# Optimization experiments

Hardware: AMD Instinct MI355X
Metric: run time of the kernel (lower is better)

## Reference

```python
import jax, jax.numpy as jnp
import numpy as np
from jax import lax

# dims: S=seq_len, B=batch, D=word dim, HE=encoder hidden, HD=decoder hidden,
# E=atomic embedding dim, A=num_atomic, T=max_steps, SOS=start token id
S, B, D = 48, 64, 300
HE, HD, E, A, T, SOS = 300, 256, 50, 128, 50, 1


def _u(key, shape, scale):
    return jax.random.uniform(key, shape, jnp.float32, -scale, scale)


def setup_inputs() -> dict:
    key = jax.random.key(0)
    ks = iter(jax.random.split(key, 64))
    inp = {"word_vectors": jax.random.normal(next(ks), (S, B, D), jnp.float32)}
    se = 1.0 / np.sqrt(HE)
    for l, din in ((0, D), (1, 2 * HE)):
        for d in ("f", "b"):
            inp[f"e{l}{d}_Wih"] = _u(next(ks), (3 * HE, din), se)
            inp[f"e{l}{d}_Whh"] = _u(next(ks), (3 * HE, HE), se)
            inp[f"e{l}{d}_bih"] = _u(next(ks), (3 * HE,), se)
            inp[f"e{l}{d}_bhh"] = _u(next(ks), (3 * HE,), se)
    sd = 1.0 / np.sqrt(HD)
    for l, din in ((0, E), (1, HD)):
        inp[f"d{l}_Wih"] = _u(next(ks), (3 * HD, din), sd)
        inp[f"d{l}_Whh"] = _u(next(ks), (3 * HD, HD), sd)
        inp[f"d{l}_bih"] = _u(next(ks), (3 * HD,), sd)
        inp[f"d{l}_bhh"] = _u(next(ks), (3 * HD,), sd)
    emb = jax.random.normal(next(ks), (A, E), jnp.float32)
    inp["emb"] = emb.at[0].set(0.0)  # padding_idx=0
    inp["Wout"] = _u(next(ks), (A, HD), sd)
    inp["bout"] = _u(next(ks), (A,), sd)
    so = 1.0 / np.sqrt(D)
    inp["Wh0"] = _u(next(ks), (2 * HD, D), so)
    inp["bh0"] = _u(next(ks), (2 * HD,), so)
    return inp


def gru_cell(x, h, Wih, Whh, bih, bhh):
    # PyTorch GRU cell semantics
    gi = x @ Wih.T + bih
    gh = h @ Whh.T + bhh
    ir, iz, inn = jnp.split(gi, 3, axis=-1)
    hr, hz, hn = jnp.split(gh, 3, axis=-1)
    r = jax.nn.sigmoid(ir + hr)
    z = jax.nn.sigmoid(iz + hz)
    n = jnp.tanh(inn + r * hn)
    return (1.0 - z) * n + z * h


def gru_layer(xs, Wih, Whh, bih, bhh, reverse=False):
    # xs: [S, B, din] -> [S, B, H]; h0 = zeros (torch default)
    h0 = jnp.zeros((xs.shape[1], Whh.shape[1]), xs.dtype)
    def step(h, x):
        hn = gru_cell(x, h, Wih, Whh, bih, bhh)
        return hn, hn
    _, ys = lax.scan(step, h0, xs, reverse=reverse)
    return ys


def reference(word_vectors, e0f_Wih, e0f_Whh, e0f_bih, e0f_bhh, e0b_Wih, e0b_Whh, e0b_bih, e0b_bhh, e1f_Wih, e1f_Whh, e1f_bih, e1f_bhh, e1b_Wih, e1b_Whh, e1b_bih, e1b_bhh, d0_Wih, d0_Whh, d0_bih, d0_bhh, d1_Wih, d1_Whh, d1_bih, d1_bhh, emb, Wout, bout, Wh0, bh0):
    # --- encoder: 2-layer bidirectional GRU (eval mode: no dropout) ---
    x0f = gru_layer(word_vectors, e0f_Wih, e0f_Whh, e0f_bih, e0f_bhh, reverse=False)
    x0b = gru_layer(word_vectors, e0b_Wih, e0b_Whh, e0b_bih, e0b_bhh, reverse=True)
    x0 = jnp.concatenate([x0f, x0b], axis=-1)  # [S,B,2*HE]
    x1f = gru_layer(x0, e1f_Wih, e1f_Whh, e1f_bih, e1f_bhh, reverse=False)
    x1b = gru_layer(x0, e1b_Wih, e1b_Whh, e1b_bih, e1b_bhh, reverse=True)
    enc = x1f + x1b  # view(S,B,2,HE).sum(dim=2) of concat == sum of directions

    N = S * B
    h = jnp.tanh(enc @ Wh0.T + bh0).reshape(N, 2, HD)  # [N,2,HD]
    h0, h1 = h[:, 0], h[:, 1]
    e = jnp.broadcast_to(emb[SOS], (N, E))

    def step(carry, _):
        h0, h1, e = carry
        h0n = gru_cell(e, h0, d0_Wih, d0_Whh, d0_bih, d0_bhh)
        h1n = gru_cell(h0n, h1, d1_Wih, d1_Whh, d1_bih, d1_bhh)
        y = jax.nn.log_softmax(h1n @ Wout.T + bout, axis=-1)  # [N,A]
        p = jnp.argmax(y, axis=-1)
        return (h0n, h1n, emb[p]), y

    _, Y = lax.scan(step, (h0, h1, e), None, length=T)  # [T,N,A]
    return Y.reshape(T, S, B, A)[:-1]
```

## Files before the change

kernel.cpp:

```cpp
#include <hip/hip_runtime.h>
#include <math.h>

#define S_ 48
#define B_ 64
#define D_ 300
#define HE_ 300
#define HD_ 256
#define E_ 50
#define A_ 128
#define T_ 50
#define N_ (S_*B_)
#define NR 6

__device__ __forceinline__ float sigm(float x){ return 1.0f/(1.0f + expf(-x)); }

template<int MODE>
__global__ __launch_bounds__(256)
void gemm_bias_kernel(const float* __restrict__ A, const float* __restrict__ W,
                      const float* __restrict__ bias, float* __restrict__ C,
                      float* __restrict__ C2, int M, int N, int K)
{
  __shared__ float As[16][64];
  __shared__ float Ws[16][64];
  const int tid = threadIdx.x;
  const int bm = blockIdx.y * 64;
  const int bn = blockIdx.x * 64;
  const int tx = tid & 15, ty = tid >> 4;
  const int lr = tid >> 2;
  const int lk = (tid & 3) << 2;
  float acc[4][4] = {{0.f}};
  for (int kb = 0; kb < K; kb += 16) {
    {
      const int row = bm + lr;
      const int k = kb + lk;
      const float* ap = A + (size_t)row * K + k;
      float4 v = make_float4(0.f,0.f,0.f,0.f);
      if (k + 3 < K) v = *reinterpret_cast<const float4*>(ap);
      else {
        if (k   < K) v.x = ap[0];
        if (k+1 < K) v.y = ap[1];
        if (k+2 < K) v.z = ap[2];
        if (k+3 < K) v.w = ap[3];
      }
      As[lk][lr]=v.x; As[lk+1][lr]=v.y; As[lk+2][lr]=v.z; As[lk+3][lr]=v.w;
    }
    {
      const int col = bn + lr;
      const int k = kb + lk;
      float4 v = make_float4(0.f,0.f,0.f,0.f);
      if (col < N) {
        const float* wp = W + (size_t)col * K + k;
        if (k + 3 < K) v = *reinterpret_cast<const float4*>(wp);
        else {
          if (k   < K) v.x = wp[0];
          if (k+1 < K) v.y = wp[1];
          if (k+2 < K) v.z = wp[2];
          if (k+3 < K) v.w = wp[3];
        }
      }
      Ws[lk][lr]=v.x; Ws[lk+1][lr]=v.y; Ws[lk+2][lr]=v.z; Ws[lk+3][lr]=v.w;
    }
    __syncthreads();
    #pragma unroll
    for (int kk = 0; kk < 16; ++kk) {
      float4 a4 = *reinterpret_cast<const float4*>(&As[kk][ty<<2]);
      float4 w4 = *reinterpret_cast<const float4*>(&Ws[kk][tx<<2]);
      const float* a = reinterpret_cast<const float*>(&a4);
      const float* w = reinterpret_cast<const float*>(&w4);
      #pragma unroll
      for (int i = 0; i < 4; ++i)
        #pragma unroll
        for (int j = 0; j < 4; ++j)
          acc[i][j] = fmaf(a[i], w[j], acc[i][j]);
    }
    __syncthreads();
  }
  #pragma unroll
  for (int i = 0; i < 4; ++i) {
    const int m = bm + (ty<<2) + i;
    #pragma unroll
    for (int j = 0; j < 4; ++j) {
      const int n = bn + (tx<<2) + j;
      if (n < N) {
        float v = acc[i][j] + bias[n];
        if (MODE == 0) {
          C[(size_t)m*N + n] = v;
        } else {
          v = tanhf(v);
          if (n < HD_) C[(size_t)m*HD_ + n] = v;
          else         C2[(size_t)m*HD_ + (n-HD_)] = v;
        }
      }
    }
  }
}

__device__ __forceinline__ void tile_mac(const float (*As)[64], const float (*Ws)[16][36],
                                         int tcol, int trow,
                                         float* accr, float* accz, float* accn)
{
  #pragma unroll
  for (int kk = 0; kk < 32; kk += 4) {
    float4 wr4 = *reinterpret_cast<const float4*>(&Ws[0][tcol][kk]);
    float4 wz4 = *reinterpret_cast<const float4*>(&Ws[1][tcol][kk]);
    float4 wn4 = *reinterpret_cast<const float4*>(&Ws[2][tcol][kk]);
    const float* wr = reinterpret_cast<const float*>(&wr4);
    const float* wz = reinterpret_cast<const float*>(&wz4);
    const float* wn = reinterpret_cast<const float*>(&wn4);
    #pragma unroll
    for (int u = 0; u < 4; ++u) {
      float4 a4 = *reinterpret_cast<const float4*>(&As[kk+u][trow]);
      const float* a = reinterpret_cast<const float*>(&a4);
      #pragma unroll
      for (int q = 0; q < 4; ++q) {
        accr[q] = fmaf(a[q], wr[u], accr[q]);
        accz[q] = fmaf(a[q], wz[u], accz[q]);
        accn[q] = fmaf(a[q], wn[u], accn[q]);
      }
    }
  }
}

__global__ __launch_bounds__(256)
void enc_step_kernel(const float* __restrict__ gi_f, const float* __restrict__ gi_b,
                     const float* __restrict__ Whh_f, const float* __restrict__ Whh_b,
                     const float* __restrict__ bhh_f, const float* __restrict__ bhh_b,
                     const float* __restrict__ hin_f, float* __restrict__ hout_f,
                     const float* __restrict__ hin_b, float* __restrict__ hout_b,
                     float* __restrict__ out, int t, int layer)
{
  const int dir = blockIdx.z;
  const float* gi  = dir ? gi_b  : gi_f;
  const float* W   = dir ? Whh_b : Whh_f;
  const float* bhh = dir ? bhh_b : bhh_f;
  const float* hin = dir ? hin_b : hin_f;
  float* hout = dir ? hout_b : hout_f;
  const int tt = dir ? (S_-1 - t) : t;

  __shared__ float As[32][64];
  __shared__ float Ws[3][16][36];
  const int tid = threadIdx.x;
  const int bn = blockIdx.x * 16;
  const int tcol = tid & 15;
  const int trow = (tid >> 4) << 2;
  float accr[4]={0,0,0,0}, accz[4]={0,0,0,0}, accn[4]={0,0,0,0};

  for (int kb = 0; kb < HE_; kb += 32) {
    __syncthreads();
    #pragma unroll
    for (int j = 0; j < 2; ++j) {
      int i = tid + j*256;
      int row = i >> 3;
      int k = (i & 7) << 2;
      const float* ap = hin + (size_t)row*HE_ + kb + k;
      float4 v = make_float4(0.f,0.f,0.f,0.f);
      if (kb + k + 3 < HE_) v = *reinterpret_cast<const float4*>(ap);
      else {
        if (kb+k   < HE_) v.x = ap[0];
        if (kb+k+1 < HE_) v.y = ap[1];
        if (kb+k+2 < HE_) v.z = ap[2];
        if (kb+k+3 < HE_) v.w = ap[3];
      }
      As[k  ][row] = v.x; As[k+1][row] = v.y; As[k+2][row] = v.z; As[k+3][row] = v.w;
    }
    #pragma unroll
    for (int j = 0; j < 6; ++j) {
      int i = tid + j*256;
      int g = i >> 9;
      int c = (i >> 5) & 15;
      int k = i & 31;
      float v = 0.0f;
      if (bn + c < HE_ && kb + k < HE_) v = W[(size_t)(g*HE_ + bn + c)*HE_ + kb + k];
      Ws[g][c][k] = v;
    }
    __syncthreads();
    tile_mac(As, Ws, tcol, trow, accr, accz, accn);
  }

  const int jcol = bn + tcol;
  if (jcol < HE_) {
    #pragma unroll
    for (int i = 0; i < 4; ++i) {
      const int row = trow + i;
      const size_t gbase = (size_t)(tt*B_ + row) * (3*HE_);
      float gr = gi[gbase + jcol];
      float gz = gi[gbase + HE_ + jcol];
      float gn = gi[gbase + 2*HE_ + jcol];
      float r = sigm(gr + accr[i] + bhh[jcol]);
      float z = sigm(gz + accz[i] + bhh[HE_ + jcol]);
      float n = tanhf(gn + r*(accn[i] + bhh[2*HE_ + jcol]));
      float ho = hin[(size_t)row*HE_ + jcol];
      float hn = (1.0f - z)*n + z*ho;
      hout[(size_t)row*HE_ + jcol] = hn;
      if (layer == 0) out[(size_t)(tt*B_ + row)*(2*HE_) + dir*HE_ + jcol] = hn;
      else            out[(size_t)(tt*B_ + row)*HE_ + jcol] += hn;
    }
  }
}

__global__ __launch_bounds__(256)
void transpose_kernel(const float* __restrict__ in, float* __restrict__ out,
                      int NC, int NK)
{
  int idx = blockIdx.x * 256 + threadIdx.x;
  if (idx < NC*NK) {
    int cI = idx / NK, kI = idx % NK;
    out[(size_t)kI*NC + cI] = in[idx];
  }
}

__global__ __launch_bounds__(512, 2)
void dec_persistent(const float* __restrict__ WihT0,
                    const float* __restrict__ WhhT0,
                    const float* __restrict__ WihT1,
                    const float* __restrict__ WhhT1,
                    const float* __restrict__ WoutT,
                    const float* __restrict__ bih0, const float* __restrict__ bhh0,
                    const float* __restrict__ bih1, const float* __restrict__ bhh1,
                    const float* __restrict__ bout,
                    const float* __restrict__ emb,
                    const float* __restrict__ h0init, const float* __restrict__ h1init,
                    float* __restrict__ Y)
{
  __shared__ float h0s[12][256];
  __shared__ float h1s[12][256];
  __shared__ float es[12][52];
  const int tid = threadIdx.x;
  const int bb = blockIdx.x;
  const int R0 = bb * 12;
  const int c  = tid & 255;
  const int half = tid >> 8;
  const int r0 = half * NR;

  for (int i = tid; i < 12*64; i += 512) {
    int r = i >> 6;
    int k = (i & 63) << 2;
    *reinterpret_cast<float4*>(&h0s[r][k]) =
        *reinterpret_cast<const float4*>(&h0init[(size_t)(R0+r)*HD_ + k]);
    *reinterpret_cast<float4*>(&h1s[r][k]) =
        *reinterpret_cast<const float4*>(&h1init[(size_t)(R0+r)*HD_ + k]);
  }
  for (int i = tid; i < 12*E_; i += 512) {
    int r = i / E_, k = i % E_;
    es[r][k] = emb[E_ + k];
  }
  const float b0r = bih0[c] + bhh0[c];
  const float b0z = bih0[HD_+c] + bhh0[HD_+c];
  const float b0ni = bih0[2*HD_+c];
  const float b0nh = bhh0[2*HD_+c];
  const float b1r = bih1[c] + bhh1[c];
  const float b1z = bih1[HD_+c] + bhh1[HD_+c];
  const float b1ni = bih1[2*HD_+c];
  const float b1nh = bhh1[2*HD_+c];
  const float bo0 = bout[tid & 63];
  const float bo1 = bout[64 + (tid & 63)];
  __syncthreads();

  for (int s = 0; s < T_-1; ++s) {
    float ar[NR], az[NR], ani[NR], anh[NR];
    #pragma unroll
    for (int r = 0; r < NR; ++r) { ar[r]=0.f; az[r]=0.f; ani[r]=0.f; anh[r]=0.f; }
    for (int k = 0; k < E_; k += 2) {
      const float* wk = WihT0 + (size_t)k*768;
      float wr0=wk[c],     wz0=wk[HD_+c],     wn0=wk[2*HD_+c];
      float wr1=wk[768+c], wz1=wk[768+HD_+c], wn1=wk[768+2*HD_+c];
      #pragma unroll
      for (int r = 0; r < NR; ++r) {
        float2 x = *reinterpret_cast<const float2*>(&es[r0+r][k]);
        ar[r]=fmaf(x.x,wr0,ar[r]);  ar[r]=fmaf(x.y,wr1,ar[r]);
        az[r]=fmaf(x.x,wz0,az[r]);  az[r]=fmaf(x.y,wz1,az[r]);
        ani[r]=fmaf(x.x,wn0,ani[r]); ani[r]=fmaf(x.y,wn1,ani[r]);
      }
    }
    for (int k = 0; k < HD_; k += 4) {
      float wr[4], wz[4], wn[4];
      #pragma unroll
      for (int u = 0; u < 4; ++u) {
        const float* wk = WhhT0 + (size_t)(k+u)*768;
        wr[u]=wk[c]; wz[u]=wk[HD_+c]; wn[u]=wk[2*HD_+c];
      }
      #pragma unroll
      for (int r = 0; r < NR; ++r) {
        float4 x = *reinterpret_cast<const float4*>(&h0s[r0+r][k]);
        ar[r]=fmaf(x.x,wr[0],ar[r]); ar[r]=fmaf(x.y,wr[1],ar[r]);
        ar[r]=fmaf(x.z,wr[2],ar[r]); ar[r]=fmaf(x.w,wr[3],ar[r]);
        az[r]=fmaf(x.x,wz[0],az[r]); az[r]=fmaf(x.y,wz[1],az[r]);
        az[r]=fmaf(x.z,wz[2],az[r]); az[r]=fmaf(x.w,wz[3],az[r]);
        anh[r]=fmaf(x.x,wn[0],anh[r]); anh[r]=fmaf(x.y,wn[1],anh[r]);
        anh[r]=fmaf(x.z,wn[2],anh[r]); anh[r]=fmaf(x.w,wn[3],anh[r]);
      }
    }
    __syncthreads();
    {
      float hnew[NR];
      #pragma unroll
      for (int r = 0; r < NR; ++r) {
        float rg = sigm(ar[r] + b0r);
        float zg = sigm(az[r] + b0z);
        float ng = tanhf(ani[r] + b0ni + rg*(anh[r] + b0nh));
        float hold = h0s[r0+r][c];
        hnew[r] = (1.0f - zg)*ng + zg*hold;
      }
      #pragma unroll
      for (int r = 0; r < NR; ++r) h0s[r0+r][c] = hnew[r];
    }
    __syncthreads();
    #pragma unroll
    for (int r = 0; r < NR; ++r) { ar[r]=0.f; az[r]=0.f; ani[r]=0.f; anh[r]=0.f; }
    for (int k = 0; k < HD_; k += 4) {
      float wr[4], wz[4], wn[4];
      #pragma unroll
      for (int u = 0; u < 4; ++u) {
        const float* wk = WihT1 + (size_t)(k+u)*768;
        wr[u]=wk[c]; wz[u]=wk[HD_+c]; wn[u]=wk[2*HD_+c];
      }
      #pragma unroll
      for (int r = 0; r < NR; ++r) {
        float4 x = *reinterpret_cast<const float4*>(&h0s[r0+r][k]);
        ar[r]=fmaf(x.x,wr[0],ar[r]); ar[r]=fmaf(x.y,wr[1],ar[r]);
        ar[r]=fmaf(x.z,wr[2],ar[r]); ar[r]=fmaf(x.w,wr[3],ar[r]);
        az[r]=fmaf(x.x,wz[0],az[r]); az[r]=fmaf(x.y,wz[1],az[r]);
        az[r]=fmaf(x.z,wz[2],az[r]); az[r]=fmaf(x.w,wz[3],az[r]);
        ani[r]=fmaf(x.x,wn[0],ani[r]); ani[r]=fmaf(x.y,wn[1],ani[r]);
        ani[r]=fmaf(x.z,wn[2],ani[r]); ani[r]=fmaf(x.w,wn[3],ani[r]);
      }
    }
    for (int k = 0; k < HD_; k += 4) {
      float wr[4], wz[4], wn[4];
      #pragma unroll
      for (int u = 0; u < 4; ++u) {
        const float* wk = WhhT1 + (size_t)(k+u)*768;
        wr[u]=wk[c]; wz[u]=wk[HD_+c]; wn[u]=wk[2*HD_+c];
      }
      #pragma unroll
      for (int r = 0; r < NR; ++r) {
        float4 x = *reinterpret_cast<const float4*>(&h1s[r0+r][k]);
        ar[r]=fmaf(x.x,wr[0],ar[r]); ar[r]=fmaf(x.y,wr[1],ar[r]);
        ar[r]=fmaf(x.z,wr[2],ar[r]); ar[r]=fmaf(x.w,wr[3],ar[r]);
        az[r]=fmaf(x.x,wz[0],az[r]); az[r]=fmaf(x.y,wz[1],az[r]);
        az[r]=fmaf(x.z,wz[2],az[r]); az[r]=fmaf(x.w,wz[3],az[r]);
        anh[r]=fmaf(x.x,wn[0],anh[r]); anh[r]=fmaf(x.y,wn[1],anh[r]);
        anh[r]=fmaf(x.z,wn[2],anh[r]); anh[r]=fmaf(x.w,wn[3],anh[r]);
      }
    }
    __syncthreads();
    {
      float hnew[NR];
      #pragma unroll
      for (int r = 0; r < NR; ++r) {
        float rg = sigm(ar[r] + b1r);
        float zg = sigm(az[r] + b1z);
        float ng = tanhf(ani[r] + b1ni + rg*(anh[r] + b1nh));
        float hold = h1s[r0+r][c];
        hnew[r] = (1.0f - zg)*ng + zg*hold;
      }
      #pragma unroll
      for (int r = 0; r < NR; ++r) h1s[r0+r][c] = hnew[r];
    }
    __syncthreads();
    {
      const int w = tid >> 6;
      const int lane = tid & 63;
      if (w < 6) {
        const int row0 = 2*w;
        float a00=0.f, a01=0.f, a10=0.f, a11=0.f;
        for (int k = 0; k < HD_; k += 2) {
          float w00 = WoutT[(size_t)k*A_ + lane];
          float w01 = WoutT[(size_t)k*A_ + 64 + lane];
          float w10 = WoutT[(size_t)(k+1)*A_ + lane];
          float w11 = WoutT[(size_t)(k+1)*A_ + 64 + lane];
          float2 hv0 = *reinterpret_cast<const float2*>(&h1s[row0][k]);
          float2 hv1 = *reinterpret_cast<const float2*>(&h1s[row0+1][k]);
          a00 = fmaf(hv0.x, w00, a00); a00 = fmaf(hv0.y, w10, a00);
          a01 = fmaf(hv0.x, w01, a01); a01 = fmaf(hv0.y, w11, a01);
          a10 = fmaf(hv1.x, w00, a10); a10 = fmaf(hv1.y, w10, a10);
          a11 = fmaf(hv1.x, w01, a11); a11 = fmaf(hv1.y, w11, a11);
        }
        float va[2][2] = {{a00,a01},{a10,a11}};
        #pragma unroll
        for (int rr = 0; rr < 2; ++rr) {
          const int row = row0 + rr;
          float v0 = va[rr][0] + bo0;
          float v1 = va[rr][1] + bo1;
          float mx = fmaxf(v0, v1);
          #pragma unroll
          for (int off = 32; off >= 1; off >>= 1) mx = fmaxf(mx, __shfl_xor(mx, off));
          float sum = expf(v0 - mx) + expf(v1 - mx);
          #pragma unroll
          for (int off = 32; off >= 1; off >>= 1) sum += __shfl_xor(sum, off);
          float lz = mx + logf(sum);
          float* Yr = Y + ((size_t)s*N_ + R0 + row)*A_;
          Yr[lane]      = v0 - lz;
          Yr[64 + lane] = v1 - lz;
          float bv; int bi;
          if (v0 >= v1) { bv = v0; bi = lane; } else { bv = v1; bi = 64 + lane; }
          #pragma unroll
          for (int off = 32; off >= 1; off >>= 1) {
            float ov = __shfl_xor(bv, off);
            int   oi = __shfl_xor(bi, off);
            if (ov > bv || (ov == bv && oi < bi)) { bv = ov; bi = oi; }
          }
          if (lane < E_) es[row][lane] = emb[(size_t)bi*E_ + lane];
        }
      }
    }
    __syncthreads();
  }
}

extern "C" void kernel_launch(void* const* d_in, const int* in_sizes, int n_in,
                              void* d_out, int out_size, void* d_ws, size_t ws_size,
                              hipStream_t stream)
{
  (void)in_sizes; (void)n_in; (void)out_size; (void)ws_size;
  const float* wv      = (const float*)d_in[0];
  const float* e0f_Wih = (const float*)d_in[1];
  const float* e0f_Whh = (const float*)d_in[2];
  const float* e0f_bih = (const float*)d_in[3];
  const float* e0f_bhh = (const float*)d_in[4];
  const float* e0b_Wih = (const float*)d_in[5];
  const float* e0b_Whh = (const float*)d_in[6];
  const float* e0b_bih = (const float*)d_in[7];
  const float* e0b_bhh = (const float*)d_in[8];
  const float* e1f_Wih = (const float*)d_in[9];
  const float* e1f_Whh = (const float*)d_in[10];
  const float* e1f_bih = (const float*)d_in[11];
  const float* e1f_bhh = (const float*)d_in[12];
  const float* e1b_Wih = (const float*)d_in[13];
  const float* e1b_Whh = (const float*)d_in[14];
  const float* e1b_bih = (const float*)d_in[15];
  const float* e1b_bhh = (const float*)d_in[16];
  const float* d0_Wih  = (const float*)d_in[17];
  const float* d0_Whh  = (const float*)d_in[18];
  const float* d0_bih  = (const float*)d_in[19];
  const float* d0_bhh  = (const float*)d_in[20];
  const float* d1_Wih  = (const float*)d_in[21];
  const float* d1_Whh  = (const float*)d_in[22];
  const float* d1_bih  = (const float*)d_in[23];
  const float* d1_bhh  = (const float*)d_in[24];
  const float* emb     = (const float*)d_in[25];
  const float* Wout    = (const float*)d_in[26];
  const float* bout    = (const float*)d_in[27];
  const float* Wh0     = (const float*)d_in[28];
  const float* bh0     = (const float*)d_in[29];

  float* ws = (float*)d_ws;
  size_t off = 0;
  auto alloc = [&](size_t n){ float* q = ws + off; off += n; return q; };
  float* giA = alloc((size_t)N_*3*HE_);
  float* giB = alloc((size_t)N_*3*HE_);
  float* x0  = alloc((size_t)N_*2*HE_);
  float* enc = alloc((size_t)N_*HE_);
  float* hfA = alloc((size_t)B_*HE_);
  float* hfB = alloc((size_t)B_*HE_);
  float* hbA = alloc((size_t)B_*HE_);
  float* hbB = alloc((size_t)B_*HE_);
  float* h0A = giA;
  float* h1A = giA + (size_t)N_*HD_;
  float* WihT0 = x0;
  float* WhhT0 = WihT0 + (size_t)E_*768;
  float* WihT1 = WhhT0 + (size_t)HD_*768;
  float* WhhT1 = WihT1 + (size_t)HD_*768;
  float* WoutT = WhhT1 + (size_t)HD_*768;
  float* Y = (float*)d_out;

  const dim3 blk(256);

  gemm_bias_kernel<0><<<dim3(15,48), blk, 0, stream>>>(wv, e0f_Wih, e0f_bih, giA, nullptr, N_, 3*HE_, D_);
  gemm_bias_kernel<0><<<dim3(15,48), blk, 0, stream>>>(wv, e0b_Wih, e0b_bih, giB, nullptr, N_, 3*HE_, D_);
  hipMemsetAsync(hfA, 0, (size_t)B_*HE_*sizeof(float), stream);
  hipMemsetAsync(hbA, 0, (size_t)B_*HE_*sizeof(float), stream);
  {
    float* hfi = hfA; float* hfo = hfB; float* hbi = hbA; float* hbo = hbB;
    for (int t = 0; t < S_; ++t) {
      enc_step_kernel<<<dim3(19,1,2), blk, 0, stream>>>(giA, giB, e0f_Whh, e0b_Whh,
          e0f_bhh, e0b_bhh, hfi, hfo, hbi, hbo, x0, t, 0);
      float* tmp = hfi; hfi = hfo; hfo = tmp;
      tmp = hbi; hbi = hbo; hbo = tmp;
    }
  }
  gemm_bias_kernel<0><<<dim3(15,48), blk, 0, stream>>>(x0, e1f_Wih, e1f_bih, giA, nullptr, N_, 3*HE_, 2*HE_);
  gemm_bias_kernel<0><<<dim3(15,48), blk, 0, stream>>>(x0, e1b_Wih, e1b_bih, giB, nullptr, N_, 3*HE_, 2*HE_);
  hipMemsetAsync(hfA, 0, (size_t)B_*HE_*sizeof(float), stream);
  hipMemsetAsync(hbA, 0, (size_t)B_*HE_*sizeof(float), stream);
  hipMemsetAsync(enc, 0, (size_t)N_*HE_*sizeof(float), stream);
  {
    float* hfi = hfA; float* hfo = hfB; float* hbi = hbA; float* hbo = hbB;
    for (int t = 0; t < S_; ++t) {
      enc_step_kernel<<<dim3(19,1,2), blk, 0, stream>>>(giA, giB, e1f_Whh, e1b_Whh,
          e1f_bhh, e1b_bhh, hfi, hfo, hbi, hbo, enc, t, 1);
      float* tmp = hfi; hfi = hfo; hfo = tmp;
      tmp = hbi; hbi = hbo; hbo = tmp;
    }
  }
  gemm_bias_kernel<1><<<dim3(8,48), blk, 0, stream>>>(enc, Wh0, bh0, h0A, h1A, N_, 2*HD_, HE_);
  transpose_kernel<<<dim3(150), blk, 0, stream>>>(d0_Wih, WihT0, 3*HD_, E_);
  transpose_kernel<<<dim3(768), blk, 0, stream>>>(d0_Whh, WhhT0, 3*HD_, HD_);
  transpose_kernel<<<dim3(768), blk, 0, stream>>>(d1_Wih, WihT1, 3*HD_, HD_);
  transpose_kernel<<<dim3(768), blk, 0, stream>>>(d1_Whh, WhhT1, 3*HD_, HD_);
  transpose_kernel<<<dim3(128), blk, 0, stream>>>(Wout,   WoutT, A_,    HD_);
  dec_persistent<<<dim3(N_/12), dim3(512), 0, stream>>>(
      WihT0, WhhT0, WihT1, WhhT1, WoutT,
      d0_bih, d0_bhh, d1_bih, d1_bhh, bout,
      emb, h0A, h1A, Y);
}
```

Measured before the change: 6.856 ms.

## Run each encoder GRU layer as one persistent kernel and merge decoder matvec loops

```diff
diff --git a/kernel.cpp b/kernel.cpp
--- a/kernel.cpp
+++ b/kernel.cpp
@@ -10,13 +10,13 @@
 #define A_ 128
 #define T_ 50
 #define N_ (S_*B_)
-#define NR 6
 
 __device__ __forceinline__ float sigm(float x){ return 1.0f/(1.0f + expf(-x)); }
 
 template<int MODE>
 __global__ __launch_bounds__(256)
-void gemm_bias_kernel(const float* __restrict__ A, const float* __restrict__ W,
+void gemm_bias_kernel(const float* __restrict__ A, const float* __restrict__ A2,
+                      const float* __restrict__ W,
                       const float* __restrict__ bias, float* __restrict__ C,
                       float* __restrict__ C2, int M, int N, int K)
 {
@@ -42,6 +42,18 @@
         if (k+2 < K) v.z = ap[2];
         if (k+3 < K) v.w = ap[3];
       }
+      if (MODE == 2) {
+        const float* ap2 = A2 + (size_t)row * K + k;
+        if (k + 3 < K) {
+          float4 v2 = *reinterpret_cast<const float4*>(ap2);
+          v.x += v2.x; v.y += v2.y; v.z += v2.z; v.w += v2.w;
+        } else {
+          if (k   < K) v.x += ap2[0];
+          if (k+1 < K) v.y += ap2[1];
+          if (k+2 < K) v.z += ap2[2];
+          if (k+3 < K) v.w += ap2[3];
+        }
+      }
       As[lk][lr]=v.x; As[lk+1][lr]=v.y; As[lk+2][lr]=v.z; As[lk+3][lr]=v.w;
     }
     {
@@ -95,121 +107,91 @@
   }
 }
 
-__device__ __forceinline__ void tile_mac(const float (*As)[64], const float (*Ws)[16][36],
-                                         int tcol, int trow,
-                                         float* accr, float* accz, float* accn)
-{
-  #pragma unroll
-  for (int kk = 0; kk < 32; kk += 4) {
-    float4 wr4 = *reinterpret_cast<const float4*>(&Ws[0][tcol][kk]);
-    float4 wz4 = *reinterpret_cast<const float4*>(&Ws[1][tcol][kk]);
-    float4 wn4 = *reinterpret_cast<const float4*>(&Ws[2][tcol][kk]);
-    const float* wr = reinterpret_cast<const float*>(&wr4);
-    const float* wz = reinterpret_cast<const float*>(&wz4);
-    const float* wn = reinterpret_cast<const float*>(&wn4);
-    #pragma unroll
-    for (int u = 0; u < 4; ++u) {
-      float4 a4 = *reinterpret_cast<const float4*>(&As[kk+u][trow]);
-      const float* a = reinterpret_cast<const float*>(&a4);
-      #pragma unroll
-      for (int q = 0; q < 4; ++q) {
-        accr[q] = fmaf(a[q], wr[u], accr[q]);
-        accz[q] = fmaf(a[q], wz[u], accz[q]);
-        accn[q] = fmaf(a[q], wn[u], accn[q]);
-      }
-    }
-  }
-}
-
-__global__ __launch_bounds__(256)
-void enc_step_kernel(const float* __restrict__ gi_f, const float* __restrict__ gi_b,
-                     const float* __restrict__ Whh_f, const float* __restrict__ Whh_b,
-                     const float* __restrict__ bhh_f, const float* __restrict__ bhh_b,
-                     const float* __restrict__ hin_f, float* __restrict__ hout_f,
-                     const float* __restrict__ hin_b, float* __restrict__ hout_b,
-                     float* __restrict__ out, int t, int layer)
-{
-  const int dir = blockIdx.z;
-  const float* gi  = dir ? gi_b  : gi_f;
-  const float* W   = dir ? Whh_b : Whh_f;
-  const float* bhh = dir ? bhh_b : bhh_f;
-  const float* hin = dir ? hin_b : hin_f;
-  float* hout = dir ? hout_b : hout_f;
-  const int tt = dir ? (S_-1 - t) : t;
-
-  __shared__ float As[32][64];
-  __shared__ float Ws[3][16][36];
-  const int tid = threadIdx.x;
-  const int bn = blockIdx.x * 16;
-  const int tcol = tid & 15;
-  const int trow = (tid >> 4) << 2;
-  float accr[4]={0,0,0,0}, accz[4]={0,0,0,0}, accn[4]={0,0,0,0};
-
-  for (int kb = 0; kb < HE_; kb += 32) {
-    __syncthreads();
-    #pragma unroll
-    for (int j = 0; j < 2; ++j) {
-      int i = tid + j*256;
-      int row = i >> 3;
-      int k = (i & 7) << 2;
-      const float* ap = hin + (size_t)row*HE_ + kb + k;
-      float4 v = make_float4(0.f,0.f,0.f,0.f);
-      if (kb + k + 3 < HE_) v = *reinterpret_cast<const float4*>(ap);
-      else {
-        if (kb+k   < HE_) v.x = ap[0];
-        if (kb+k+1 < HE_) v.y = ap[1];
-        if (kb+k+2 < HE_) v.z = ap[2];
-        if (kb+k+3 < HE_) v.w = ap[3];
-      }
-      As[k  ][row] = v.x; As[k+1][row] = v.y; As[k+2][row] = v.z; As[k+3][row] = v.w;
-    }
-    #pragma unroll
-    for (int j = 0; j < 6; ++j) {
-      int i = tid + j*256;
-      int g = i >> 9;
-      int c = (i >> 5) & 15;
-      int k = i & 31;
-      float v = 0.0f;
-      if (bn + c < HE_ && kb + k < HE_) v = W[(size_t)(g*HE_ + bn + c)*HE_ + kb + k];
-      Ws[g][c][k] = v;
-    }
-    __syncthreads();
-    tile_mac(As, Ws, tcol, trow, accr, accz, accn);
-  }
-
-  const int jcol = bn + tcol;
-  if (jcol < HE_) {
-    #pragma unroll
-    for (int i = 0; i < 4; ++i) {
-      const int row = trow + i;
-      const size_t gbase = (size_t)(tt*B_ + row) * (3*HE_);
-      float gr = gi[gbase + jcol];
-      float gz = gi[gbase + HE_ + jcol];
-      float gn = gi[gbase + 2*HE_ + jcol];
-      float r = sigm(gr + accr[i] + bhh[jcol]);
-      float z = sigm(gz + accz[i] + bhh[HE_ + jcol]);
-      float n = tanhf(gn + r*(accn[i] + bhh[2*HE_ + jcol]));
-      float ho = hin[(size_t)row*HE_ + jcol];
-      float hn = (1.0f - z)*n + z*ho;
-      hout[(size_t)row*HE_ + jcol] = hn;
-      if (layer == 0) out[(size_t)(tt*B_ + row)*(2*HE_) + dir*HE_ + jcol] = hn;
-      else            out[(size_t)(tt*B_ + row)*HE_ + jcol] += hn;
-    }
-  }
-}
-
 __global__ __launch_bounds__(256)
 void transpose_kernel(const float* __restrict__ in, float* __restrict__ out,
-                      int NC, int NK)
+                      int NC, int NK, int NKP)
 {
   int idx = blockIdx.x * 256 + threadIdx.x;
-  if (idx < NC*NK) {
-    int cI = idx / NK, kI = idx % NK;
-    out[(size_t)kI*NC + cI] = in[idx];
+  if (idx < NC*NKP) {
+    int cI = idx / NKP, kI = idx % NKP;
+    out[(size_t)kI*NC + cI] = (kI < NK) ? in[(size_t)cI*NK + kI] : 0.0f;
   }
 }
 
-__global__ __launch_bounds__(512, 2)
+template<int LAYER>
+__global__ __launch_bounds__(640)
+void enc_layer_persistent(const float* __restrict__ gi_f, const float* __restrict__ gi_b,
+                          const float* __restrict__ WhhT_f, const float* __restrict__ WhhT_b,
+                          const float* __restrict__ bhh_f, const float* __restrict__ bhh_b,
+                          float* __restrict__ out, float* __restrict__ outB)
+{
+  const int dir = blockIdx.y;
+  const float* gi  = dir ? gi_b   : gi_f;
+  const float* WT  = dir ? WhhT_b : WhhT_f;
+  const float* bhh = dir ? bhh_b  : bhh_f;
+  float* o = (LAYER == 1 && dir) ? outB : out;
+
+  __shared__ float hA[8][304];
+  __shared__ float hB[8][304];
+  const int tid = threadIdx.x;
+  const int half = tid / 320;
+  const int j = tid - half*320;
+  const int R0 = blockIdx.x * 8;
+  const int r0 = half * 4;
+  const bool act = (j < HE_);
+
+  float b_r = 0.f, b_z = 0.f, b_n = 0.f;
+  if (act) { b_r = bhh[j]; b_z = bhh[HE_+j]; b_n = bhh[2*HE_+j]; }
+  __syncthreads();
+
+  for (int t = 0; t < S_; ++t) {
+    const int tt = dir ? (S_-1 - t) : t;
+    float (*hin)[304]  = (t & 1) ? hB : hA;
+    float (*hout)[304] = (t & 1) ? hA : hB;
+    float ar[4]={0,0,0,0}, az[4]={0,0,0,0}, an[4]={0,0,0,0};
+    if (act && t > 0) {
+      for (int k = 0; k < HE_; k += 4) {
+        float wr[4], wz[4], wn[4];
+        #pragma unroll
+        for (int u = 0; u < 4; ++u) {
+          const float* wk = WT + (size_t)(k+u)*(3*HE_);
+          wr[u] = wk[j]; wz[u] = wk[HE_+j]; wn[u] = wk[2*HE_+j];
+        }
+        #pragma unroll
+        for (int r = 0; r < 4; ++r) {
+          float4 h4 = *reinterpret_cast<const float4*>(&hin[r0+r][k]);
+          ar[r]=fmaf(h4.x,wr[0],ar[r]); ar[r]=fmaf(h4.y,wr[1],ar[r]);
+          ar[r]=fmaf(h4.z,wr[2],ar[r]); ar[r]=fmaf(h4.w,wr[3],ar[r]);
+          az[r]=fmaf(h4.x,wz[0],az[r]); az[r]=fmaf(h4.y,wz[1],az[r]);
+          az[r]=fmaf(h4.z,wz[2],az[r]); az[r]=fmaf(h4.w,wz[3],az[r]);
+          an[r]=fmaf(h4.x,wn[0],an[r]); an[r]=fmaf(h4.y,wn[1],an[r]);
+          an[r]=fmaf(h4.z,wn[2],an[r]); an[r]=fmaf(h4.w,wn[3],an[r]);
+        }
+      }
+    }
+    if (act) {
+      #pragma unroll
+      for (int r = 0; r < 4; ++r) {
+        const int row = R0 + r0 + r;
+        const size_t gb = (size_t)(tt*B_ + row) * (3*HE_);
+        float gr = gi[gb + j];
+        float gz = gi[gb + HE_ + j];
+        float gn = gi[gb + 2*HE_ + j];
+        float rg = sigm(gr + ar[r] + b_r);
+        float zg = sigm(gz + az[r] + b_z);
+        float ng = tanhf(gn + rg*(an[r] + b_n));
+        float ho = (t > 0) ? hin[r0+r][j] : 0.0f;
+        float hn = (1.0f - zg)*ng + zg*ho;
+        hout[r0+r][j] = hn;
+        if (LAYER == 0) o[(size_t)(tt*B_ + row)*(2*HE_) + dir*HE_ + j] = hn;
+        else            o[(size_t)(tt*B_ + row)*HE_ + j] = hn;
+      }
+    }
+    __syncthreads();
+  }
+}
+
+__global__ __launch_bounds__(512)
 void dec_persistent(const float* __restrict__ WihT0,
                     const float* __restrict__ WhhT0,
                     const float* __restrict__ WihT1,
@@ -226,23 +208,21 @@
   __shared__ float h1s[12][256];
   __shared__ float es[12][52];
   const int tid = threadIdx.x;
-  const int bb = blockIdx.x;
-  const int R0 = bb * 12;
+  const int R0 = blockIdx.x * 12;
   const int c  = tid & 255;
   const int half = tid >> 8;
-  const int r0 = half * NR;
+  const int r0 = half * 6;
 
   for (int i = tid; i < 12*64; i += 512) {
-    int r = i >> 6;
-    int k = (i & 63) << 2;
+    int r = i >> 6, k = (i & 63) << 2;
     *reinterpret_cast<float4*>(&h0s[r][k]) =
         *reinterpret_cast<const float4*>(&h0init[(size_t)(R0+r)*HD_ + k]);
     *reinterpret_cast<float4*>(&h1s[r][k]) =
         *reinterpret_cast<const float4*>(&h1init[(size_t)(R0+r)*HD_ + k]);
   }
-  for (int i = tid; i < 12*E_; i += 512) {
-    int r = i / E_, k = i % E_;
-    es[r][k] = emb[E_ + k];
+  for (int i = tid; i < 12*52; i += 512) {
+    int r = i / 52, k = i - r*52;
+    es[r][k] = (k < E_) ? emb[E_ + k] : 0.0f;
   }
   const float b0r = bih0[c] + bhh0[c];
   const float b0z = bih0[HD_+c] + bhh0[HD_+c];
@@ -257,30 +237,18 @@
   __syncthreads();
 
   for (int s = 0; s < T_-1; ++s) {
-    float ar[NR], az[NR], ani[NR], anh[NR];
-    #pragma unroll
-    for (int r = 0; r < NR; ++r) { ar[r]=0.f; az[r]=0.f; ani[r]=0.f; anh[r]=0.f; }
-    for (int k = 0; k < E_; k += 2) {
-      const float* wk = WihT0 + (size_t)k*768;
-      float wr0=wk[c],     wz0=wk[HD_+c],     wn0=wk[2*HD_+c];
-      float wr1=wk[768+c], wz1=wk[768+HD_+c], wn1=wk[768+2*HD_+c];
-      #pragma unroll
-      for (int r = 0; r < NR; ++r) {
-        float2 x = *reinterpret_cast<const float2*>(&es[r0+r][k]);
-        ar[r]=fmaf(x.x,wr0,ar[r]);  ar[r]=fmaf(x.y,wr1,ar[r]);
-        az[r]=fmaf(x.x,wz0,az[r]);  az[r]=fmaf(x.y,wz1,az[r]);
-        ani[r]=fmaf(x.x,wn0,ani[r]); ani[r]=fmaf(x.y,wn1,ani[r]);
-      }
-    }
-    for (int k = 0; k < HD_; k += 4) {
+    float ar[6]={0,0,0,0,0,0}, az[6]={0,0,0,0,0,0};
+    float ani[6]={0,0,0,0,0,0}, anh[6]={0,0,0,0,0,0};
+    for (int kq = 0; kq < 64; ++kq) {
+      const int k = kq << 2;
       float wr[4], wz[4], wn[4];
       #pragma unroll
       for (int u = 0; u < 4; ++u) {
         const float* wk = WhhT0 + (size_t)(k+u)*768;
-        wr[u]=wk[c]; wz[u]=wk[HD_+c]; wn[u]=wk[2*HD_+c];
-      }
-      #pragma unroll
-      for (int r = 0; r < NR; ++r) {
+        wr[u]=wk[c]; wz[u]=wk[256+c]; wn[u]=wk[512+c];
+      }
+      #pragma unroll
+      for (int r = 0; r < 6; ++r) {
         float4 x = *reinterpret_cast<const float4*>(&h0s[r0+r][k]);
         ar[r]=fmaf(x.x,wr[0],ar[r]); ar[r]=fmaf(x.y,wr[1],ar[r]);
         ar[r]=fmaf(x.z,wr[2],ar[r]); ar[r]=fmaf(x.w,wr[3],ar[r]);
@@ -289,12 +257,30 @@
         anh[r]=fmaf(x.x,wn[0],anh[r]); anh[r]=fmaf(x.y,wn[1],anh[r]);
         anh[r]=fmaf(x.z,wn[2],anh[r]); anh[r]=fmaf(x.w,wn[3],anh[r]);
       }
+      if (kq < 13) {
+        float vr[4], vz[4], vn[4];
+        #pragma unroll
+        for (int u = 0; u < 4; ++u) {
+          const float* wk = WihT0 + (size_t)(k+u)*768;
+          vr[u]=wk[c]; vz[u]=wk[256+c]; vn[u]=wk[512+c];
+        }
+        #pragma unroll
+        for (int r = 0; r < 6; ++r) {
+          float4 e = *reinterpret_cast<const float4*>(&es[r0+r][k]);
+          ar[r]=fmaf(e.x,vr[0],ar[r]); ar[r]=fmaf(e.y,vr[1],ar[r]);
+          ar[r]=fmaf(e.z,vr[2],ar[r]); ar[r]=fmaf(e.w,vr[3],ar[r]);
+          az[r]=fmaf(e.x,vz[0],az[r]); az[r]=fmaf(e.y,vz[1],az[r]);
+          az[r]=fmaf(e.z,vz[2],az[r]); az[r]=fmaf(e.w,vz[3],az[r]);
+          ani[r]=fmaf(e.x,vn[0],ani[r]); ani[r]=fmaf(e.y,vn[1],ani[r]);
+          ani[r]=fmaf(e.z,vn[2],ani[r]); ani[r]=fmaf(e.w,vn[3],ani[r]);
+        }
+      }
     }
     __syncthreads();
     {
-      float hnew[NR];
-      #pragma unroll
-      for (int r = 0; r < NR; ++r) {
+      float hnew[6];
+      #pragma unroll
+      for (int r = 0; r < 6; ++r) {
         float rg = sigm(ar[r] + b0r);
         float zg = sigm(az[r] + b0z);
         float ng = tanhf(ani[r] + b0ni + rg*(anh[r] + b0nh));
@@ -302,52 +288,44 @@
         hnew[r] = (1.0f - zg)*ng + zg*hold;
       }
       #pragma unroll
-      for (int r = 0; r < NR; ++r) h0s[r0+r][c] = hnew[r];
+      for (int r = 0; r < 6; ++r) h0s[r0+r][c] = hnew[r];
     }
     __syncthreads();
     #pragma unroll
-    for (int r = 0; r < NR; ++r) { ar[r]=0.f; az[r]=0.f; ani[r]=0.f; anh[r]=0.f; }
-    for (int k = 0; k < HD_; k += 4) {
-      float wr[4], wz[4], wn[4];
+    for (int r = 0; r < 6; ++r) { ar[r]=0.f; az[r]=0.f; ani[r]=0.f; anh[r]=0.f; }
+    for (int kq = 0; kq < 64; ++kq) {
+      const int k = kq << 2;
+      float vr[4], vz[4], vn[4], wr[4], wz[4], wn[4];
       #pragma unroll
       for (int u = 0; u < 4; ++u) {
-        const float* wk = WihT1 + (size_t)(k+u)*768;
-        wr[u]=wk[c]; wz[u]=wk[HD_+c]; wn[u]=wk[2*HD_+c];
-      }
-      #pragma unroll
-      for (int r = 0; r < NR; ++r) {
+        const float* wk  = WihT1 + (size_t)(k+u)*768;
+        vr[u]=wk[c]; vz[u]=wk[256+c]; vn[u]=wk[512+c];
+        const float* wk2 = WhhT1 + (size_t)(k+u)*768;
+        wr[u]=wk2[c]; wz[u]=wk2[256+c]; wn[u]=wk2[512+c];
+      }
+      #pragma unroll
+      for (int r = 0; r < 6; ++r) {
         float4 x = *reinterpret_cast<const float4*>(&h0s[r0+r][k]);
-        ar[r]=fmaf(x.x,wr[0],ar[r]); ar[r]=fmaf(x.y,wr[1],ar[r]);
-        ar[r]=fmaf(x.z,wr[2],ar[r]); ar[r]=fmaf(x.w,wr[3],ar[r]);
-        az[r]=fmaf(x.x,wz[0],az[r]); az[r]=fmaf(x.y,wz[1],az[r]);
-        az[r]=fmaf(x.z,wz[2],az[r]); az[r]=fmaf(x.w,wz[3],az[r]);
-        ani[r]=fmaf(x.x,wn[0],ani[r]); ani[r]=fmaf(x.y,wn[1],ani[r]);
-        ani[r]=fmaf(x.z,wn[2],ani[r]); ani[r]=fmaf(x.w,wn[3],ani[r]);
-      }
-    }
-    for (int k = 0; k < HD_; k += 4) {
-      float wr[4], wz[4], wn[4];
-      #pragma unroll
-      for (int u = 0; u < 4; ++u) {
-        const float* wk = WhhT1 + (size_t)(k+u)*768;
-        wr[u]=wk[c]; wz[u]=wk[HD_+c]; wn[u]=wk[2*HD_+c];
-      }
-      #pragma unroll
-      for (int r = 0; r < NR; ++r) {
-        float4 x = *reinterpret_cast<const float4*>(&h1s[r0+r][k]);
-        ar[r]=fmaf(x.x,wr[0],ar[r]); ar[r]=fmaf(x.y,wr[1],ar[r]);
-        ar[r]=fmaf(x.z,wr[2],ar[r]); ar[r]=fmaf(x.w,wr[3],ar[r]);
-        az[r]=fmaf(x.x,wz[0],az[r]); az[r]=fmaf(x.y,wz[1],az[r]);
-        az[r]=fmaf(x.z,wz[2],az[r]); az[r]=fmaf(x.w,wz[3],az[r]);
-        anh[r]=fmaf(x.x,wn[0],anh[r]); anh[r]=fmaf(x.y,wn[1],anh[r]);
-        anh[r]=fmaf(x.z,wn[2],anh[r]); anh[r]=fmaf(x.w,wn[3],anh[r]);
+        ar[r]=fmaf(x.x,vr[0],ar[r]); ar[r]=fmaf(x.y,vr[1],ar[r]);
+        ar[r]=fmaf(x.z,vr[2],ar[r]); ar[r]=fmaf(x.w,vr[3],ar[r]);
+        az[r]=fmaf(x.x,vz[0],az[r]); az[r]=fmaf(x.y,vz[1],az[r]);
+        az[r]=fmaf(x.z,vz[2],az[r]); az[r]=fmaf(x.w,vz[3],az[r]);
+        ani[r]=fmaf(x.x,vn[0],ani[r]); ani[r]=fmaf(x.y,vn[1],ani[r]);
+        ani[r]=fmaf(x.z,vn[2],ani[r]); ani[r]=fmaf(x.w,vn[3],ani[r]);
+        float4 y = *reinterpret_cast<const float4*>(&h1s[r0+r][k]);
+        ar[r]=fmaf(y.x,wr[0],ar[r]); ar[r]=fmaf(y.y,wr[1],ar[r]);
+        ar[r]=fmaf(y.z,wr[2],ar[r]); ar[r]=fmaf(y.w,wr[3],ar[r]);
+        az[r]=fmaf(y.x,wz[0],az[r]); az[r]=fmaf(y.y,wz[1],az[r]);
+        az[r]=fmaf(y.z,wz[2],az[r]); az[r]=fmaf(y.w,wz[3],az[r]);
+        anh[r]=fmaf(y.x,wn[0],anh[r]); anh[r]=fmaf(y.y,wn[1],anh[r]);
+        anh[r]=fmaf(y.z,wn[2],anh[r]); anh[r]=fmaf(y.w,wn[3],anh[r]);
       }
     }
     __syncthreads();
     {
-      float hnew[NR];
-      #pragma unroll
-      for (int r = 0; r < NR; ++r) {
+      float hnew[6];
+      #pragma unroll
+      for (int r = 0; r < 6; ++r) {
         float rg = sigm(ar[r] + b1r);
         float zg = sigm(az[r] + b1z);
         float ng = tanhf(ani[r] + b1ni + rg*(anh[r] + b1nh));
@@ -355,7 +333,7 @@
         hnew[r] = (1.0f - zg)*ng + zg*hold;
       }
       #pragma unroll
-      for (int r = 0; r < NR; ++r) h1s[r0+r][c] = hnew[r];
+      for (int r = 0; r < 6; ++r) h1s[r0+r][c] = hnew[r];
     }
     __syncthreads();
     {
@@ -445,20 +423,20 @@
   const float* bh0     = (const float*)d_in[29];
 
   float* ws = (float*)d_ws;
-  size_t off = 0;
-  auto alloc = [&](size_t n){ float* q = ws + off; off += n; return q; };
-  float* giA = alloc((size_t)N_*3*HE_);
-  float* giB = alloc((size_t)N_*3*HE_);
-  float* x0  = alloc((size_t)N_*2*HE_);
-  float* enc = alloc((size_t)N_*HE_);
-  float* hfA = alloc((size_t)B_*HE_);
-  float* hfB = alloc((size_t)B_*HE_);
-  float* hbA = alloc((size_t)B_*HE_);
-  float* hbB = alloc((size_t)B_*HE_);
-  float* h0A = giA;
-  float* h1A = giA + (size_t)N_*HD_;
-  float* WihT0 = x0;
-  float* WhhT0 = WihT0 + (size_t)E_*768;
+  float* giA  = ws;
+  float* giB  = giA + (size_t)N_*3*HE_;
+  float* x0   = giB + (size_t)N_*3*HE_;
+  float* eWhT = x0  + (size_t)N_*2*HE_;
+  float* eT0f = eWhT;
+  float* eT0b = eT0f + (size_t)3*HE_*HE_;
+  float* eT1f = eT0b + (size_t)3*HE_*HE_;
+  float* eT1b = eT1f + (size_t)3*HE_*HE_;
+  float* encF = x0;
+  float* encB = x0 + (size_t)N_*HE_;
+  float* h0A  = giA;
+  float* h1A  = giA + (size_t)N_*HD_;
+  float* WihT0 = eWhT;
+  float* WhhT0 = WihT0 + (size_t)52*768;
   float* WihT1 = WhhT0 + (size_t)HD_*768;
   float* WhhT1 = WihT1 + (size_t)HD_*768;
   float* WoutT = WhhT1 + (size_t)HD_*768;
@@ -466,39 +444,22 @@
 
   const dim3 blk(256);
 
-  gemm_bias_kernel<0><<<dim3(15,48), blk, 0, stream>>>(wv, e0f_Wih, e0f_bih, giA, nullptr, N_, 3*HE_, D_);
-  gemm_bias_kernel<0><<<dim3(15,48), blk, 0, stream>>>(wv, e0b_Wih, e0b_bih, giB, nullptr, N_, 3*HE_, D_);
-  hipMemsetAsync(hfA, 0, (size_t)B_*HE_*sizeof(float), stream);
-  hipMemsetAsync(hbA, 0, (size_t)B_*HE_*sizeof(float), stream);
-  {
-    float* hfi = hfA; float* hfo = hfB; float* hbi = hbA; float* hbo = hbB;
-    for (int t = 0; t < S_; ++t) {
-      enc_step_kernel<<<dim3(19,1,2), blk, 0, stream>>>(giA, giB, e0f_Whh, e0b_Whh,
-          e0f_bhh, e0b_bhh, hfi, hfo, hbi, hbo, x0, t, 0);
-      float* tmp = hfi; hfi = hfo; hfo = tmp;
-      tmp = hbi; hbi = hbo; hbo = tmp;
-    }
-  }
-  gemm_bias_kernel<0><<<dim3(15,48), blk, 0, stream>>>(x0, e1f_Wih, e1f_bih, giA, nullptr, N_, 3*HE_, 2*HE_);
-  gemm_bias_kernel<0><<<dim3(15,48), blk, 0, stream>>>(x0, e1b_Wih, e1b_bih, giB, nullptr, N_, 3*HE_, 2*HE_);
-  hipMemsetAsync(hfA, 0, (size_t)B_*HE_*sizeof(float), stream);
-  hipMemsetAsync(hbA, 0, (size_t)B_*HE_*sizeof(float), stream);
-  hipMemsetAsync(enc, 0, (size_t)N_*HE_*sizeof(float), stream);
-  {
-    float* hfi = hfA; float* hfo = hfB; float* hbi = hbA; float* hbo = hbB;
-    for (int t = 0; t < S_; ++t) {
-      enc_step_kernel<<<dim3(19,1,2), blk, 0, stream>>>(giA, giB, e1f_Whh, e1b_Whh,
-          e1f_bhh, e1b_bhh, hfi, hfo, hbi, hbo, enc, t, 1);
-      float* tmp = hfi; hfi = hfo; hfo = tmp;
-      tmp = hbi; hbi = hbo; hbo = tmp;
-    }
-  }
-  gemm_bias_kernel<1><<<dim3(8,48), blk, 0, stream>>>(enc, Wh0, bh0, h0A, h1A, N_, 2*HD_, HE_);
-  transpose_kernel<<<dim3(150), blk, 0, stream>>>(d0_Wih, WihT0, 3*HD_, E_);
-  transpose_kernel<<<dim3(768), blk, 0, stream>>>(d0_Whh, WhhT0, 3*HD_, HD_);
-  transpose_kernel<<<dim3(768), blk, 0, stream>>>(d1_Wih, WihT1, 3*HD_, HD_);
-  transpose_kernel<<<dim3(768), blk, 0, stream>>>(d1_Whh, WhhT1, 3*HD_, HD_);
-  transpose_kernel<<<dim3(128), blk, 0, stream>>>(Wout,   WoutT, A_,    HD_);
+  transpose_kernel<<<dim3((3*HE_*HE_+255)/256), blk, 0, stream>>>(e0f_Whh, eT0f, 3*HE_, HE_, HE_);
+  transpose_kernel<<<dim3((3*HE_*HE_+255)/256), blk, 0, stream>>>(e0b_Whh, eT0b, 3*HE_, HE_, HE_);
+  transpose_kernel<<<dim3((3*HE_*HE_+255)/256), blk, 0, stream>>>(e1f_Whh, eT1f, 3*HE_, HE_, HE_);
+  transpose_kernel<<<dim3((3*HE_*HE_+255)/256), blk, 0, stream>>>(e1b_Whh, eT1b, 3*HE_, HE_, HE_);
+  gemm_bias_kernel<0><<<dim3(15,48), blk, 0, stream>>>(wv, nullptr, e0f_Wih, e0f_bih, giA, nullptr, N_, 3*HE_, D_);
+  gemm_bias_kernel<0><<<dim3(15,48), blk, 0, stream>>>(wv, nullptr, e0b_Wih, e0b_bih, giB, nullptr, N_, 3*HE_, D_);
+  enc_layer_persistent<0><<<dim3(8,2), dim3(640), 0, stream>>>(giA, giB, eT0f, eT0b, e0f_bhh, e0b_bhh, x0, nullptr);
+  gemm_bias_kernel<0><<<dim3(15,48), blk, 0, stream>>>(x0, nullptr, e1f_Wih, e1f_bih, giA, nullptr, N_, 3*HE_, 2*HE_);
+  gemm_bias_kernel<0><<<dim3(15,48), blk, 0, stream>>>(x0, nullptr, e1b_Wih, e1b_bih, giB, nullptr, N_, 3*HE_, 2*HE_);
+  enc_layer_persistent<1><<<dim3(8,2), dim3(640), 0, stream>>>(giA, giB, eT1f, eT1b, e1f_bhh, e1b_bhh, encF, encB);
+  transpose_kernel<<<dim3((768*52+255)/256),   blk, 0, stream>>>(d0_Wih, WihT0, 3*HD_, E_,  52);
+  transpose_kernel<<<dim3((768*256+255)/256),  blk, 0, stream>>>(d0_Whh, WhhT0, 3*HD_, HD_, HD_);
+  transpose_kernel<<<dim3((768*256+255)/256),  blk, 0, stream>>>(d1_Wih, WihT1, 3*HD_, HD_, HD_);
+  transpose_kernel<<<dim3((768*256+255)/256),  blk, 0, stream>>>(d1_Whh, WhhT1, 3*HD_, HD_, HD_);
+  transpose_kernel<<<dim3((128*256+255)/256),  blk, 0, stream>>>(Wout,   WoutT, A_,    HD_, HD_);
+  gemm_bias_kernel<2><<<dim3(8,48), blk, 0, stream>>>(encF, encB, Wh0, bh0, h0A, h1A, N_, 2*HD_, HE_);
   dec_persistent<<<dim3(N_/12), dim3(512), 0, stream>>>(
       WihT0, WhhT0, WihT1, WhhT1, WoutT,
       d0_bih, d0_bhh, d1_bih, d1_bhh, bout,
```

Measured after the change: 7.835 ms. 14.3% more time.
